# Kernel optimization log

Measured on AMD Instinct MI355X. Metric: run time of the kernel, lower is better.

The kernel has to match this reference:

```python
import jax, jax.numpy as jnp
import numpy as np

N = 100000   # skill_num
D = 128      # skill_embed_dim
E = 500000   # edges per relation
S = 16384    # queried skills
NEG_SLOPE = 0.2


def _gat(x, edge_index, W, att_src, att_dst, bias):
    # PyG GATConv, heads=1, add_self_loops=True, eval mode (no dropout)
    n = x.shape[0]
    loops = jnp.arange(n)
    src = jnp.concatenate([edge_index[0], loops])
    dst = jnp.concatenate([edge_index[1], loops])
    h = x @ W                              # [N, D]
    a_src = h @ att_src                    # [N]
    a_dst = h @ att_dst                    # [N]
    e = jax.nn.leaky_relu(a_src[src] + a_dst[dst], NEG_SLOPE)  # [E+N]
    emax = jax.ops.segment_max(e, dst, num_segments=n)
    ex = jnp.exp(e - emax[dst])
    denom = jax.ops.segment_sum(ex, dst, num_segments=n)
    alpha = ex / (denom[dst] + 1e-16)
    out = jax.ops.segment_sum(alpha[:, None] * h[src], dst, num_segments=n)
    return out + bias


def _sage(x, edge_index, Wl, bl, Wr):
    # PyG SAGEConv, aggr='mean', root_weight=True (lin_r has no bias)
    n = x.shape[0]
    src, dst = edge_index[0], edge_index[1]
    ones = jnp.ones((src.shape[0],), dtype=x.dtype)
    deg = jax.ops.segment_sum(ones, dst, num_segments=n)
    agg = jax.ops.segment_sum(x[src], dst, num_segments=n)
    agg = agg / jnp.maximum(deg, 1.0)[:, None]
    return agg @ Wl + bl + x @ Wr


def setup_inputs() -> dict:
    key = jax.random.key(0)
    ks = jax.random.split(key, 16)
    sc = 1.0 / np.sqrt(D)
    inp = {
        "s": jax.random.randint(ks[0], (S,), 0, N),
        "t_s": 0,
        "t_e": 12,
        "ei_parent": jax.random.randint(ks[1], (2, E), 0, N),
        "ei_child": jax.random.randint(ks[2], (2, E), 0, N),
        "ei_relate": jax.random.randint(ks[3], (2, E), 0, N),
        "emb": jax.random.normal(ks[4], (N, D), dtype=jnp.float32),
        # GAT is_parent params
        "Wp": jax.random.normal(ks[5], (D, D), dtype=jnp.float32) * sc,
        "asp": jax.random.normal(ks[6], (D,), dtype=jnp.float32) * sc,
        "adp": jax.random.normal(ks[7], (D,), dtype=jnp.float32) * sc,
        "bp": jnp.zeros((D,), dtype=jnp.float32),
        # GAT is_child params
        "Wc": jax.random.normal(ks[8], (D, D), dtype=jnp.float32) * sc,
        "asc": jax.random.normal(ks[9], (D,), dtype=jnp.float32) * sc,
        "adc": jax.random.normal(ks[10], (D,), dtype=jnp.float32) * sc,
        "bc": jnp.zeros((D,), dtype=jnp.float32),
        # SAGE relate params
        "Wl": jax.random.normal(ks[11], (D, D), dtype=jnp.float32) * sc,
        "bl": jnp.zeros((D,), dtype=jnp.float32),
        "Wr": jax.random.normal(ks[12], (D, D), dtype=jnp.float32) * sc,
    }
    return inp


def reference(s, t_s, t_e, ei_parent, ei_child, ei_relate, emb,
              Wp, asp, adp, bp, Wc, asc, adc, bc, Wl, bl, Wr):
    out_parent = _gat(emb, ei_parent, Wp, asp, adp, bp)
    out_child = _gat(emb, ei_child, Wc, asc, adc, bc)
    out_relate = _sage(emb, ei_relate, Wl, bl, Wr)
    # HeteroConv(aggr='mean') over the three relation outputs
    node_out = (out_parent + out_child + out_relate) / 3.0
    return node_out[s, :]
```

## Files before the change

kernel.cpp:

```cpp
#include <hip/hip_runtime.h>

#define D 128
#define CAP 64
#define OVF_CAP 1024

typedef short bf16x8 __attribute__((ext_vector_type(8)));
typedef float f32x4 __attribute__((ext_vector_type(4)));

__device__ __forceinline__ unsigned short f2bf(float f) {
  unsigned u = __builtin_bit_cast(unsigned, f);
  unsigned r = (u + 0x7fffu + ((u >> 16) & 1u)) >> 16;
  return (unsigned short)r;
}
__device__ __forceinline__ float bflo(unsigned r) {
  return __builtin_bit_cast(float, r << 16);
}
__device__ __forceinline__ float bfhi(unsigned r) {
  return __builtin_bit_cast(float, r & 0xffff0000u);
}
__device__ __forceinline__ float lrelu(float t) {
  return t >= 0.f ? t : 0.2f * t;
}


__global__ void k_setup(const float* __restrict__ Wp, const float* __restrict__ asp,
                        const float* __restrict__ adp, const float* __restrict__ Wc,
                        const float* __restrict__ asc, const float* __restrict__ adc,
                        const float* __restrict__ bp, const float* __restrict__ bc,
                        const float* __restrict__ bl, const float* __restrict__ Wl,
                        const float* __restrict__ Wr,
                        float* __restrict__ v, unsigned short* __restrict__ wpack,
                        int* __restrict__ qid, int* __restrict__ counters,
                        int* __restrict__ deg3, int N, int S3) {
  int i = blockIdx.x * blockDim.x + threadIdx.x;
  int stride = gridDim.x * blockDim.x;
  for (int k = i; k < N; k += stride) qid[k] = -1;
  for (int k = i; k < S3; k += stride) deg3[k] = 0;
  if (i < 16) counters[i] = 0;

  for (int idx = i; idx < 16 * 8 * 64 * 8; idx += stride) {
    int j    = idx & 7;
    int lane = (idx >> 3) & 63;
    int nt   = (idx >> 9) & 7;
    int kt   = idx >> 12;
    int o = kt >> 2;
    int c = (kt & 3) * 32 + (lane >> 4) * 8 + j;
    int n = nt * 16 + (lane & 15);
    const float* W = (o == 0) ? Wp : (o == 1) ? Wc : (o == 2) ? Wl : Wr;
    wpack[idx] = f2bf(W[c * D + n]);
  }

  if (blockIdx.x == 0 && threadIdx.x < 128) {
    int k = threadIdx.x;
    float s0 = 0.f, s1 = 0.f, s2 = 0.f, s3 = 0.f;
    for (int d = 0; d < D; ++d) {
      float wp = Wp[k * D + d], wc = Wc[k * D + d];
      s0 += wp * asp[d]; s1 += wp * adp[d];
      s2 += wc * asc[d]; s3 += wc * adc[d];
    }
    v[k] = s0; v[D + k] = s1; v[2 * D + k] = s2; v[3 * D + k] = s3;
    v[4 * D + k] = bp[k] + bc[k] + bl[k];
  }
}

__global__ void k_pre(const int* __restrict__ s, int* __restrict__ qid,
                      int* __restrict__ uniq, int* __restrict__ counters, int S,
                      const float* __restrict__ emb, const float* __restrict__ v,
                      float* __restrict__ a_sp, float* __restrict__ a_dp,
                      float* __restrict__ a_sc, float* __restrict__ a_dc,
                      unsigned* __restrict__ ebf, int N) {
  int gtid = blockIdx.x * blockDim.x + threadIdx.x;
  if (gtid < S) {
    int n = s[gtid];
    if (atomicCAS(&qid[n], -1, -2) == -1) {
      int u = atomicAdd(&counters[0], 1);
      uniq[u] = n;
      qid[n] = u;
    }
  }
  int lane = threadIdx.x & 63;
  int node = (gtid >> 6) * 2 + (lane >> 5);
  int c = lane & 31;
  if (node >= N) return;
  float4 x4 = ((const float4*)(emb + (size_t)node * D))[c];
  uint2 p;
  p.x = ((unsigned)f2bf(x4.x)) | (((unsigned)f2bf(x4.y)) << 16);
  p.y = ((unsigned)f2bf(x4.z)) | (((unsigned)f2bf(x4.w)) << 16);
  ((uint2*)ebf)[(size_t)node * 32 + c] = p;
  float4 v0 = ((const float4*)(v))[c];
  float4 v1 = ((const float4*)(v + D))[c];
  float4 v2 = ((const float4*)(v + 2 * D))[c];
  float4 v3 = ((const float4*)(v + 3 * D))[c];
  float s0 = x4.x * v0.x + x4.y * v0.y + x4.z * v0.z + x4.w * v0.w;
  float s1 = x4.x * v1.x + x4.y * v1.y + x4.z * v1.z + x4.w * v1.w;
  float s2 = x4.x * v2.x + x4.y * v2.y + x4.z * v2.z + x4.w * v2.w;
  float s3 = x4.x * v3.x + x4.y * v3.y + x4.z * v3.z + x4.w * v3.w;
#pragma unroll
  for (int o = 16; o > 0; o >>= 1) {
    s0 += __shfl_down(s0, o);
    s1 += __shfl_down(s1, o);
    s2 += __shfl_down(s2, o);
    s3 += __shfl_down(s3, o);
  }
  if (c == 0) { a_sp[node] = s0; a_dp[node] = s1; a_sc[node] = s2; a_dc[node] = s3; }
}

__global__ void __launch_bounds__(256) k_filter(
    const int* __restrict__ eiP, const int* __restrict__ eiC, const int* __restrict__ eiR,
    const int* __restrict__ qid,
    int* __restrict__ bktP, int* __restrict__ bktC, int* __restrict__ bktR,
    int* __restrict__ degP, int* __restrict__ degC, int* __restrict__ degR,
    int2* __restrict__ ovf, int* __restrict__ counters, int E) {
  int rel = blockIdx.y;
  const int* ei = (rel == 0) ? eiP : (rel == 1) ? eiC : eiR;
  int* bkt      = (rel == 0) ? bktP : (rel == 1) ? bktC : bktR;
  int* deg      = (rel == 0) ? degP : (rel == 1) ? degC : degR;
  int e = blockIdx.x * 256 + threadIdx.x;
  if (e >= E) return;
  int dst = ei[E + e];
  int u = qid[dst];
  if (u < 0) return;
  int src = ei[e];
  int pos = atomicAdd(&deg[u], 1);
  if (pos < CAP) {
    bkt[u * CAP + pos] = src;
  } else {
    int o = atomicAdd(&counters[4 + rel], 1);
    if (o < OVF_CAP) { int2 t; t.x = src; t.y = u; ovf[rel * OVF_CAP + o] = t; }
  }
}

__global__ void __launch_bounds__(256) k_fused(
    const int* __restrict__ bktP, const int* __restrict__ bktC, const int* __restrict__ bktR,
    const int* __restrict__ degP, const int* __restrict__ degC, const int* __restrict__ degR,
    const float* __restrict__ a_sp, const float* __restrict__ a_dp,
    const float* __restrict__ a_sc, const float* __restrict__ a_dc,
    const unsigned* __restrict__ ebf, const float* __restrict__ emb,
    const int* __restrict__ uniq, const int* __restrict__ counters,
    const int2* __restrict__ ovf, const float* __restrict__ vvec,
    const unsigned short* __restrict__ wpack, float* __restrict__ outU) {
  __shared__ unsigned short A_lds[16 * 64 * 8];
  int U = counters[0];
  int u0 = blockIdx.x * 16;
  if (u0 >= U) return;
  int tid = threadIdx.x;
  int w = tid >> 6;
  int lane = tid & 63;

  const int* bkts[3] = {bktP, bktC, bktR};
  const int* degs[3] = {degP, degC, degR};
  int Lc[3];
#pragma unroll
  for (int r = 0; r < 3; ++r) {
    int L = counters[4 + r];
    Lc[r] = (L > OVF_CAP) ? OVF_CAP : L;
  }

  for (int t = 0; t < 4; ++t) {
    int m = 4 * w + t;
    int u = u0 + m;
    float2 z[4];
    if (u < U) {
      int n = uniq[u];
      float2 x2 = ((const float2*)(emb + (size_t)n * D))[lane];
      float2 acc[3];
      float den[2];
#pragma unroll
      for (int r = 0; r < 3; ++r) {
        int dg = degs[r][u];
        int mc = (dg < CAP) ? dg : CAP;
        const int* b0 = bkts[r] + u * CAP;
        int srcl = (lane < mc) ? b0[lane] : 0;
        float wl = 0.f;
        float adn = 0.f;
        const float* a_s = (r == 0) ? a_sp : a_sc;
        if (r < 2) {
          adn = ((r == 0) ? a_dp : a_dc)[n];
          if (lane < mc) wl = __expf(lrelu(a_s[srcl] + adn));
        } else {
          wl = (lane < mc) ? 1.f : 0.f;
        }
        float2 a; a.x = 0.f; a.y = 0.f;
        int i = 0;
        for (; i + 4 <= mc; i += 4) {
          int s0 = __shfl(srcl, i),     s1 = __shfl(srcl, i + 1);
          int s2 = __shfl(srcl, i + 2), s3 = __shfl(srcl, i + 3);
          float w0 = __shfl(wl, i),     w1 = __shfl(wl, i + 1);
          float w2 = __shfl(wl, i + 2), w3 = __shfl(wl, i + 3);
          unsigned r0 = ebf[(size_t)s0 * 64 + lane];
          unsigned r1 = ebf[(size_t)s1 * 64 + lane];
          unsigned r2 = ebf[(size_t)s2 * 64 + lane];
          unsigned r3 = ebf[(size_t)s3 * 64 + lane];
          a.x += w0 * bflo(r0) + w1 * bflo(r1) + w2 * bflo(r2) + w3 * bflo(r3);
          a.y += w0 * bfhi(r0) + w1 * bfhi(r1) + w2 * bfhi(r2) + w3 * bfhi(r3);
        }
        for (; i < mc; ++i) {
          int si = __shfl(srcl, i);
          float wi = __shfl(wl, i);
          unsigned rr = ebf[(size_t)si * 64 + lane];
          a.x += wi * bflo(rr);
          a.y += wi * bfhi(rr);
        }
        float denx = 0.f;
        if (dg > CAP) {
          for (int l = 0; l < Lc[r]; ++l) {
            int2 ov = ovf[r * OVF_CAP + l];
            if (ov.y == u) {
              float wv = 1.f;
              if (r < 2) wv = __expf(lrelu(a_s[ov.x] + adn));
              unsigned rr = ebf[(size_t)ov.x * 64 + lane];
              a.x += wv * bflo(rr);
              a.y += wv * bfhi(rr);
              denx += wv;
            }
          }
        }
        if (r < 2) {
          float dsum = wl;
#pragma unroll
          for (int o = 32; o > 0; o >>= 1) dsum += __shfl_down(dsum, o);
          den[r] = __shfl(dsum, 0) + denx;
        } else {
          float dgc = (float)dg; if (dgc < 1.f) dgc = 1.f;
          a.x *= (1.f / dgc); a.y *= (1.f / dgc);
        }
        acc[r] = a;
      }
      float wP = __expf(lrelu(a_sp[n] + a_dp[n]));
      float rP = 1.f / (den[0] + wP);
      float wC = __expf(lrelu(a_sc[n] + a_dc[n]));
      float rC = 1.f / (den[1] + wC);
      z[0].x = (acc[0].x + wP * x2.x) * rP; z[0].y = (acc[0].y + wP * x2.y) * rP;
      z[1].x = (acc[1].x + wC * x2.x) * rC; z[1].y = (acc[1].y + wC * x2.y) * rC;
      z[2] = acc[2];
      z[3] = x2;
    } else {
      z[0].x = 0.f; z[0].y = 0.f; z[1] = z[0]; z[2] = z[0]; z[3] = z[0];
    }
    int ktc = lane >> 4;
    int q = (lane >> 2) & 3;
    int j0 = 2 * (lane & 3);
#pragma unroll
    for (int o = 0; o < 4; ++o) {
      int kt = o * 4 + ktc;
      unsigned pk = ((unsigned)f2bf(z[o].x)) | (((unsigned)f2bf(z[o].y)) << 16);
      *(unsigned*)&A_lds[(kt * 64 + q * 16 + m) * 8 + j0] = pk;
    }
  }
  __syncthreads();

  f32x4 acc0 = {0.f, 0.f, 0.f, 0.f};
  f32x4 acc1 = {0.f, 0.f, 0.f, 0.f};
  const bf16x8* wp = (const bf16x8*)wpack;
#pragma unroll
  for (int kt = 0; kt < 16; ++kt) {
    bf16x8 a  = *(const bf16x8*)&A_lds[(kt * 64 + lane) * 8];
    bf16x8 b0 = wp[(kt * 8 + 2 * w) * 64 + lane];
    bf16x8 b1 = wp[(kt * 8 + 2 * w + 1) * 64 + lane];
    acc0 = __builtin_amdgcn_mfma_f32_16x16x32_bf16(a, b0, acc0, 0, 0, 0);
    acc1 = __builtin_amdgcn_mfma_f32_16x16x32_bf16(a, b1, acc1, 0, 0, 0);
  }

  int col0 = 2 * w * 16 + (lane & 15);
  int col1 = col0 + 16;
  int r0 = (lane >> 4) * 4;
  float b0v = vvec[4 * D + col0] * (1.f / 3.f);
  float b1v = vvec[4 * D + col1] * (1.f / 3.f);
#pragma unroll
  for (int reg = 0; reg < 4; ++reg) {
    int u = u0 + r0 + reg;
    if (u < U) {
      outU[(size_t)u * D + col0] = acc0[reg] * (1.f / 3.f) + b0v;
      outU[(size_t)u * D + col1] = acc1[reg] * (1.f / 3.f) + b1v;
    }
  }
}

__global__ void k_gather(const int* __restrict__ s, const int* __restrict__ qid,
                         const float* __restrict__ outU, float* __restrict__ out, int S) {
  int idx = blockIdx.x * blockDim.x + threadIdx.x;
  if (idx >= S * D) return;
  int i = idx >> 7;
  int d = idx & (D - 1);
  int u = qid[s[i]];
  out[idx] = outU[(size_t)u * D + d];
}


extern "C" void kernel_launch(void* const* d_in, const int* in_sizes, int n_in,
                              void* d_out, int out_size, void* d_ws, size_t ws_size,
                              hipStream_t stream) {
  const int*   s   = (const int*)d_in[0];
  const int*   eip = (const int*)d_in[3];
  const int*   eic = (const int*)d_in[4];
  const int*   eir = (const int*)d_in[5];
  const float* emb = (const float*)d_in[6];
  const float* Wp  = (const float*)d_in[7];
  const float* asp = (const float*)d_in[8];
  const float* adp = (const float*)d_in[9];
  const float* bp  = (const float*)d_in[10];
  const float* Wc  = (const float*)d_in[11];
  const float* asc = (const float*)d_in[12];
  const float* adc = (const float*)d_in[13];
  const float* bc  = (const float*)d_in[14];
  const float* Wl  = (const float*)d_in[15];
  const float* bl  = (const float*)d_in[16];
  const float* Wr  = (const float*)d_in[17];
  float* out = (float*)d_out;

  const int S = in_sizes[0];
  const int E = in_sizes[3] / 2;
  const int N = in_sizes[6] / D;

  char* base = (char*)d_ws;
  size_t off = 0;
  auto carve = [&](size_t bytes) -> char* {
    char* q = base + off;
    off += (bytes + 255) & ~(size_t)255;
    return q;
  };
  float*    a_sp     = (float*)carve((size_t)N * 4);
  float*    a_dp     = (float*)carve((size_t)N * 4);
  float*    a_sc     = (float*)carve((size_t)N * 4);
  float*    a_dc     = (float*)carve((size_t)N * 4);
  int*      qid      = (int*)carve((size_t)N * 4);
  unsigned* ebf      = (unsigned*)carve((size_t)N * 64 * 4);
  int*      uniq     = (int*)carve((size_t)S * 4);
  int*      counters = (int*)carve(64);
  float*    vvec     = (float*)carve(5 * D * 4);
  unsigned short* wpack = (unsigned short*)carve((size_t)16 * 8 * 64 * 8 * 2);
  float*    outU     = (float*)carve((size_t)S * D * 4);
  int*      degP     = (int*)carve((size_t)S * 4);
  int*      degC     = (int*)carve((size_t)S * 4);
  int*      degR     = (int*)carve((size_t)S * 4);
  int*      bktP     = (int*)carve((size_t)S * CAP * 4);
  int*      bktC     = (int*)carve((size_t)S * CAP * 4);
  int*      bktR     = (int*)carve((size_t)S * CAP * 4);
  int2*     ovf      = (int2*)carve((size_t)3 * OVF_CAP * 8);
  (void)ws_size; (void)n_in; (void)out_size;

  k_setup<<<256, 256, 0, stream>>>(Wp, asp, adp, Wc, asc, adc, bp, bc, bl, Wl, Wr,
                                   vvec, wpack, qid, counters, degP, N, 3 * S);

  k_pre<<<(N * 32 + 255) / 256, 256, 0, stream>>>(s, qid, uniq, counters, S,
                                                  emb, vvec, a_sp, a_dp, a_sc, a_dc,
                                                  ebf, N);

  k_filter<<<dim3((E + 255) / 256, 3), 256, 0, stream>>>(
      eip, eic, eir, qid, bktP, bktC, bktR, degP, degC, degR, ovf, counters, E);

  k_fused<<<(S + 15) / 16, 256, 0, stream>>>(
      bktP, bktC, bktR, degP, degC, degR,
      a_sp, a_dp, a_sc, a_dc, ebf, emb, uniq, counters, ovf,
      vvec, wpack, outU);

  k_gather<<<(S * D + 255) / 256, 256, 0, stream>>>(s, qid, outU, out, S);
}
```

Baseline: 198.4 us.

## Precompute GAT edge weights and denominators during edge filtering, restructure fused kernel

The filter kernel now computes each kept edge's attention weight exp(lrelu(a_src+a_dst)). It stores the weight next to the source index in the bucket and atomically adds it into a per-node denominator. That removes the dependent a_src gather, the exp and the wave reductions from the fused kernel. Self-loop weights are precomputed per node in the pre kernel, and unique-node assignment uses a wave-aggregated atomic. The fused kernel moves to 512 threads with one 16-column MFMA tile per wave, processes two nodes per wave, and uses an XOR-swizzled LDS layout to cut bank conflicts. In exchange, bucket storage for the two GAT relations doubles in width, and float atomics make the denominators order-nondeterministic.

```diff
diff --git a/kernel.cpp b/kernel.cpp
--- a/kernel.cpp
+++ b/kernel.cpp
@@ -21,6 +21,7 @@
 __device__ __forceinline__ float lrelu(float t) {
   return t >= 0.f ? t : 0.2f * t;
 }
+__device__ __forceinline__ int swz(int b) { return b ^ (((b >> 8) & 7) << 4); }
 
 
 __global__ void k_setup(const float* __restrict__ Wp, const float* __restrict__ asp,
@@ -31,11 +32,11 @@
                         const float* __restrict__ Wr,
                         float* __restrict__ v, unsigned short* __restrict__ wpack,
                         int* __restrict__ qid, int* __restrict__ counters,
-                        int* __restrict__ deg3, int N, int S3) {
+                        int* __restrict__ deg5, int N, int S5) {
   int i = blockIdx.x * blockDim.x + threadIdx.x;
   int stride = gridDim.x * blockDim.x;
   for (int k = i; k < N; k += stride) qid[k] = -1;
-  for (int k = i; k < S3; k += stride) deg3[k] = 0;
+  for (int k = i; k < S5; k += stride) deg5[k] = 0;
   if (i < 16) counters[i] = 0;
 
   for (int idx = i; idx < 16 * 8 * 64 * 8; idx += stride) {
@@ -68,17 +69,26 @@
                       const float* __restrict__ emb, const float* __restrict__ v,
                       float* __restrict__ a_sp, float* __restrict__ a_dp,
                       float* __restrict__ a_sc, float* __restrict__ a_dc,
+                      float* __restrict__ selfP, float* __restrict__ selfC,
                       unsigned* __restrict__ ebf, int N) {
   int gtid = blockIdx.x * blockDim.x + threadIdx.x;
+  int lane = threadIdx.x & 63;
   if (gtid < S) {
     int n = s[gtid];
-    if (atomicCAS(&qid[n], -1, -2) == -1) {
-      int u = atomicAdd(&counters[0], 1);
-      uniq[u] = n;
-      qid[n] = u;
-    }
-  }
-  int lane = threadIdx.x & 63;
+    bool won = (atomicCAS(&qid[n], -1, -2) == -1);
+    unsigned long long mask = __ballot(won);
+    if (mask != 0ull) {
+      int leader = __builtin_ctzll(mask);
+      int base = 0;
+      if (lane == leader) base = atomicAdd(&counters[0], __popcll(mask));
+      base = __shfl(base, leader);
+      if (won) {
+        int u = base + __popcll(mask & ((1ull << lane) - 1ull));
+        uniq[u] = n;
+        qid[n] = u;
+      }
+    }
+  }
   int node = (gtid >> 6) * 2 + (lane >> 5);
   int c = lane & 31;
   if (node >= N) return;
@@ -102,44 +112,68 @@
     s2 += __shfl_down(s2, o);
     s3 += __shfl_down(s3, o);
   }
-  if (c == 0) { a_sp[node] = s0; a_dp[node] = s1; a_sc[node] = s2; a_dc[node] = s3; }
+  if (c == 0) {
+    a_sp[node] = s0; a_dp[node] = s1; a_sc[node] = s2; a_dc[node] = s3;
+    selfP[node] = __expf(lrelu(s0 + s1));
+    selfC[node] = __expf(lrelu(s2 + s3));
+  }
 }
 
 __global__ void __launch_bounds__(256) k_filter(
-    const int* __restrict__ eiP, const int* __restrict__ eiC, const int* __restrict__ eiR,
-    const int* __restrict__ qid,
-    int* __restrict__ bktP, int* __restrict__ bktC, int* __restrict__ bktR,
+    const int* __restrict__ eiP, const int* __restrict__ eiC,
+    const int* __restrict__ eiR, const int* __restrict__ qid,
+    int2* __restrict__ bktP, int2* __restrict__ bktC, int* __restrict__ bktR,
     int* __restrict__ degP, int* __restrict__ degC, int* __restrict__ degR,
+    float* __restrict__ denP, float* __restrict__ denC,
+    const float* __restrict__ a_sp, const float* __restrict__ a_dp,
+    const float* __restrict__ a_sc, const float* __restrict__ a_dc,
     int2* __restrict__ ovf, int* __restrict__ counters, int E) {
   int rel = blockIdx.y;
   const int* ei = (rel == 0) ? eiP : (rel == 1) ? eiC : eiR;
-  int* bkt      = (rel == 0) ? bktP : (rel == 1) ? bktC : bktR;
-  int* deg      = (rel == 0) ? degP : (rel == 1) ? degC : degR;
   int e = blockIdx.x * 256 + threadIdx.x;
   if (e >= E) return;
   int dst = ei[E + e];
   int u = qid[dst];
   if (u < 0) return;
   int src = ei[e];
+  int* deg = (rel == 0) ? degP : (rel == 1) ? degC : degR;
   int pos = atomicAdd(&deg[u], 1);
-  if (pos < CAP) {
-    bkt[u * CAP + pos] = src;
+  if (rel == 2) {
+    if (pos < CAP) {
+      bktR[u * CAP + pos] = src;
+    } else {
+      int o = atomicAdd(&counters[6], 1);
+      if (o < OVF_CAP) { int2 tt; tt.x = src; tt.y = u; ovf[2 * OVF_CAP + o] = tt; }
+    }
   } else {
-    int o = atomicAdd(&counters[4 + rel], 1);
-    if (o < OVF_CAP) { int2 t; t.x = src; t.y = u; ovf[rel * OVF_CAP + o] = t; }
-  }
-}
-
-__global__ void __launch_bounds__(256) k_fused(
-    const int* __restrict__ bktP, const int* __restrict__ bktC, const int* __restrict__ bktR,
-    const int* __restrict__ degP, const int* __restrict__ degC, const int* __restrict__ degR,
+    const float* a_s = (rel == 0) ? a_sp : a_sc;
+    const float* a_d = (rel == 0) ? a_dp : a_dc;
+    float wgt = __expf(lrelu(a_s[src] + a_d[dst]));
+    atomicAdd((rel == 0) ? &denP[u] : &denC[u], wgt);
+    if (pos < CAP) {
+      int2 tt; tt.x = src; tt.y = __builtin_bit_cast(int, wgt);
+      ((rel == 0) ? bktP : bktC)[u * CAP + pos] = tt;
+    } else {
+      int o = atomicAdd(&counters[4 + rel], 1);
+      if (o < OVF_CAP) { int2 tt; tt.x = src; tt.y = u; ovf[rel * OVF_CAP + o] = tt; }
+    }
+  }
+}
+
+__global__ void __launch_bounds__(512, 4) k_fused(
+    const int2* __restrict__ bktP, const int2* __restrict__ bktC,
+    const int* __restrict__ bktR,
+    const int* __restrict__ degP, const int* __restrict__ degC,
+    const int* __restrict__ degR,
+    const float* __restrict__ denP, const float* __restrict__ denC,
     const float* __restrict__ a_sp, const float* __restrict__ a_dp,
     const float* __restrict__ a_sc, const float* __restrict__ a_dc,
+    const float* __restrict__ selfP, const float* __restrict__ selfC,
     const unsigned* __restrict__ ebf, const float* __restrict__ emb,
     const int* __restrict__ uniq, const int* __restrict__ counters,
     const int2* __restrict__ ovf, const float* __restrict__ vvec,
     const unsigned short* __restrict__ wpack, float* __restrict__ outU) {
-  __shared__ unsigned short A_lds[16 * 64 * 8];
+  __shared__ __align__(16) unsigned short A_lds[16 * 64 * 8];
   int U = counters[0];
   int u0 = blockIdx.x * 16;
   if (u0 >= U) return;
@@ -147,8 +181,6 @@
   int w = tid >> 6;
   int lane = tid & 63;
 
-  const int* bkts[3] = {bktP, bktC, bktR};
-  const int* degs[3] = {degP, degC, degR};
   int Lc[3];
 #pragma unroll
   for (int r = 0; r < 3; ++r) {
@@ -156,29 +188,28 @@
     Lc[r] = (L > OVF_CAP) ? OVF_CAP : L;
   }
 
-  for (int t = 0; t < 4; ++t) {
-    int m = 4 * w + t;
+#pragma unroll
+  for (int t = 0; t < 2; ++t) {
+    int m = 2 * w + t;
     int u = u0 + m;
     float2 z[4];
     if (u < U) {
       int n = uniq[u];
       float2 x2 = ((const float2*)(emb + (size_t)n * D))[lane];
-      float2 acc[3];
-      float den[2];
 #pragma unroll
       for (int r = 0; r < 3; ++r) {
-        int dg = degs[r][u];
+        int dg = ((r == 0) ? degP : (r == 1) ? degC : degR)[u];
         int mc = (dg < CAP) ? dg : CAP;
-        const int* b0 = bkts[r] + u * CAP;
-        int srcl = (lane < mc) ? b0[lane] : 0;
+        int srcl = 0;
         float wl = 0.f;
-        float adn = 0.f;
-        const float* a_s = (r == 0) ? a_sp : a_sc;
         if (r < 2) {
-          adn = ((r == 0) ? a_dp : a_dc)[n];
-          if (lane < mc) wl = __expf(lrelu(a_s[srcl] + adn));
+          if (lane < mc) {
+            int2 sw_ = ((r == 0) ? bktP : bktC)[u * CAP + lane];
+            srcl = sw_.x;
+            wl = __builtin_bit_cast(float, sw_.y);
+          }
         } else {
-          wl = (lane < mc) ? 1.f : 0.f;
+          if (lane < mc) { srcl = bktR[u * CAP + lane]; wl = 1.f; }
         }
         float2 a; a.x = 0.f; a.y = 0.f;
         int i = 0;
@@ -201,8 +232,9 @@
           a.x += wi * bflo(rr);
           a.y += wi * bfhi(rr);
         }
-        float denx = 0.f;
         if (dg > CAP) {
+          const float* a_s = (r == 0) ? a_sp : a_sc;
+          float adn = (r == 0) ? a_dp[n] : (r == 1) ? a_dc[n] : 0.f;
           for (int l = 0; l < Lc[r]; ++l) {
             int2 ov = ovf[r * OVF_CAP + l];
             if (ov.y == u) {
@@ -211,28 +243,22 @@
               unsigned rr = ebf[(size_t)ov.x * 64 + lane];
               a.x += wv * bflo(rr);
               a.y += wv * bfhi(rr);
-              denx += wv;
             }
           }
         }
-        if (r < 2) {
-          float dsum = wl;
-#pragma unroll
-          for (int o = 32; o > 0; o >>= 1) dsum += __shfl_down(dsum, o);
-          den[r] = __shfl(dsum, 0) + denx;
-        } else {
+        if (r == 2) {
           float dgc = (float)dg; if (dgc < 1.f) dgc = 1.f;
-          a.x *= (1.f / dgc); a.y *= (1.f / dgc);
-        }
-        acc[r] = a;
+          float rc = 1.f / dgc;
+          a.x *= rc; a.y *= rc;
+        }
+        z[r] = a;
       }
-      float wP = __expf(lrelu(a_sp[n] + a_dp[n]));
-      float rP = 1.f / (den[0] + wP);
-      float wC = __expf(lrelu(a_sc[n] + a_dc[n]));
-      float rC = 1.f / (den[1] + wC);
-      z[0].x = (acc[0].x + wP * x2.x) * rP; z[0].y = (acc[0].y + wP * x2.y) * rP;
-      z[1].x = (acc[1].x + wC * x2.x) * rC; z[1].y = (acc[1].y + wC * x2.y) * rC;
-      z[2] = acc[2];
+      float wP = selfP[n];
+      float rP = 1.f / (denP[u] + wP);
+      float wC = selfC[n];
+      float rC = 1.f / (denC[u] + wC);
+      z[0].x = (z[0].x + wP * x2.x) * rP; z[0].y = (z[0].y + wP * x2.y) * rP;
+      z[1].x = (z[1].x + wC * x2.x) * rC; z[1].y = (z[1].y + wC * x2.y) * rC;
       z[3] = x2;
     } else {
       z[0].x = 0.f; z[0].y = 0.f; z[1] = z[0]; z[2] = z[0]; z[3] = z[0];
@@ -244,35 +270,28 @@
     for (int o = 0; o < 4; ++o) {
       int kt = o * 4 + ktc;
       unsigned pk = ((unsigned)f2bf(z[o].x)) | (((unsigned)f2bf(z[o].y)) << 16);
-      *(unsigned*)&A_lds[(kt * 64 + q * 16 + m) * 8 + j0] = pk;
+      int off = ((kt * 64 + q * 16 + m) * 8 + j0) * 2;
+      *(unsigned*)((char*)A_lds + swz(off)) = pk;
     }
   }
   __syncthreads();
 
-  f32x4 acc0 = {0.f, 0.f, 0.f, 0.f};
-  f32x4 acc1 = {0.f, 0.f, 0.f, 0.f};
+  f32x4 acc = {0.f, 0.f, 0.f, 0.f};
   const bf16x8* wp = (const bf16x8*)wpack;
 #pragma unroll
   for (int kt = 0; kt < 16; ++kt) {
-    bf16x8 a  = *(const bf16x8*)&A_lds[(kt * 64 + lane) * 8];
-    bf16x8 b0 = wp[(kt * 8 + 2 * w) * 64 + lane];
-    bf16x8 b1 = wp[(kt * 8 + 2 * w + 1) * 64 + lane];
-    acc0 = __builtin_amdgcn_mfma_f32_16x16x32_bf16(a, b0, acc0, 0, 0, 0);
-    acc1 = __builtin_amdgcn_mfma_f32_16x16x32_bf16(a, b1, acc1, 0, 0, 0);
-  }
-
-  int col0 = 2 * w * 16 + (lane & 15);
-  int col1 = col0 + 16;
+    bf16x8 a = *(const bf16x8*)((const char*)A_lds + swz((kt * 64 + lane) * 16));
+    bf16x8 b = wp[(kt * 8 + w) * 64 + lane];
+    acc = __builtin_amdgcn_mfma_f32_16x16x32_bf16(a, b, acc, 0, 0, 0);
+  }
+
+  int col = w * 16 + (lane & 15);
   int r0 = (lane >> 4) * 4;
-  float b0v = vvec[4 * D + col0] * (1.f / 3.f);
-  float b1v = vvec[4 * D + col1] * (1.f / 3.f);
+  float bv = vvec[4 * D + col] * (1.f / 3.f);
 #pragma unroll
   for (int reg = 0; reg < 4; ++reg) {
     int u = u0 + r0 + reg;
-    if (u < U) {
-      outU[(size_t)u * D + col0] = acc0[reg] * (1.f / 3.f) + b0v;
-      outU[(size_t)u * D + col1] = acc1[reg] * (1.f / 3.f) + b1v;
-    }
+    if (u < U) outU[(size_t)u * D + col] = acc[reg] * (1.f / 3.f) + bv;
   }
 }
 
@@ -323,6 +342,8 @@
   float*    a_dp     = (float*)carve((size_t)N * 4);
   float*    a_sc     = (float*)carve((size_t)N * 4);
   float*    a_dc     = (float*)carve((size_t)N * 4);
+  float*    selfP    = (float*)carve((size_t)N * 4);
+  float*    selfC    = (float*)carve((size_t)N * 4);
   int*      qid      = (int*)carve((size_t)N * 4);
   unsigned* ebf      = (unsigned*)carve((size_t)N * 64 * 4);
   int*      uniq     = (int*)carve((size_t)S * 4);
@@ -333,25 +354,28 @@
   int*      degP     = (int*)carve((size_t)S * 4);
   int*      degC     = (int*)carve((size_t)S * 4);
   int*      degR     = (int*)carve((size_t)S * 4);
-  int*      bktP     = (int*)carve((size_t)S * CAP * 4);
-  int*      bktC     = (int*)carve((size_t)S * CAP * 4);
+  float*    denP     = (float*)carve((size_t)S * 4);
+  float*    denC     = (float*)carve((size_t)S * 4);
+  int2*     bktP     = (int2*)carve((size_t)S * CAP * 8);
+  int2*     bktC     = (int2*)carve((size_t)S * CAP * 8);
   int*      bktR     = (int*)carve((size_t)S * CAP * 4);
   int2*     ovf      = (int2*)carve((size_t)3 * OVF_CAP * 8);
   (void)ws_size; (void)n_in; (void)out_size;
 
   k_setup<<<256, 256, 0, stream>>>(Wp, asp, adp, Wc, asc, adc, bp, bc, bl, Wl, Wr,
-                                   vvec, wpack, qid, counters, degP, N, 3 * S);
+                                   vvec, wpack, qid, counters, degP, N, 5 * S);
 
   k_pre<<<(N * 32 + 255) / 256, 256, 0, stream>>>(s, qid, uniq, counters, S,
                                                   emb, vvec, a_sp, a_dp, a_sc, a_dc,
-                                                  ebf, N);
+                                                  selfP, selfC, ebf, N);
 
   k_filter<<<dim3((E + 255) / 256, 3), 256, 0, stream>>>(
-      eip, eic, eir, qid, bktP, bktC, bktR, degP, degC, degR, ovf, counters, E);
-
-  k_fused<<<(S + 15) / 16, 256, 0, stream>>>(
-      bktP, bktC, bktR, degP, degC, degR,
-      a_sp, a_dp, a_sc, a_dc, ebf, emb, uniq, counters, ovf,
+      eip, eic, eir, qid, bktP, bktC, bktR, degP, degC, degR, denP, denC,
+      a_sp, a_dp, a_sc, a_dc, ovf, counters, E);
+
+  k_fused<<<(S + 15) / 16, 512, 0, stream>>>(
+      bktP, bktC, bktR, degP, degC, degR, denP, denC,
+      a_sp, a_dp, a_sc, a_dc, selfP, selfC, ebf, emb, uniq, counters, ovf,
       vvec, wpack, outU);
 
   k_gather<<<(S * D + 255) / 256, 256, 0, stream>>>(s, qid, outU, out, S);
```

Result: no change. 195.8 us (-1.3%).
